# Performance work log

Hardware: AMD Instinct MI355X
Metric: run time of the kernel (lower is better)

The kernel has to match this reference:

```python
import jax, jax.numpy as jnp
import numpy as np


def setup_inputs() -> dict:
    key = jax.random.key(0)
    # coeffs_tensor: stacked/padded wavelet coefficients [B, F, T]
    coeffs = jax.random.normal(key, (16, 256, 8192), dtype=jnp.float32)
    return {"coeffs": coeffs}


def reference(coeffs) -> jnp.ndarray:
    B, F, T = coeffs.shape
    # torch.angle on a real tensor -> 0 for x>=0, pi for x<0; jnp.angle matches.
    phase = jnp.angle(coeffs)
    inst_freq = jnp.diff(phase, axis=-1)
    inst_freq = jnp.pad(inst_freq, ((0, 0), (0, 0), (0, 1)))  # F.pad(..., (0,1))
    freq_adjusted = jnp.clip(inst_freq, -1.0, 1.0)  # [B,F,T]
    # k = (f + freq_adjusted).long(); .long() truncates toward zero, as does astype(int32)
    f_idx = jnp.arange(F, dtype=coeffs.dtype)[None, :, None]
    k = jnp.clip((f_idx + freq_adjusted).astype(jnp.int32), 0, F - 1)  # [B,F,T]
    # Fused scatter-add over all (b, f, t): sst[b, k[b,f,t], t] += coeffs[b, f, t]
    b_idx = jnp.arange(B)[:, None, None]
    t_idx = jnp.arange(T)[None, None, :]
    sst = jnp.zeros_like(coeffs).at[b_idx, k, t_idx].add(coeffs)
    return sst
```

## Files before the change

### kernel.cpp

```cpp
#include <hip/hip_runtime.h>

#define BB 16
#define FF 256
#define TT 8192
#define F_CHUNK 16
#define THREADS 256

__device__ __forceinline__ int sgn_bit(float x) {
    return (int)(__float_as_uint(x) >> 31);
}

struct Raw { float4 v; float e; };

__global__ __launch_bounds__(THREADS) void sst_kernel(const float* __restrict__ in,
                                                      float* __restrict__ out) {
    const int t    = blockIdx.x * (THREADS * 4) + threadIdx.x * 4;
    const int fs   = blockIdx.y * F_CHUNK;
    const int b    = blockIdx.z;
    const int lane = threadIdx.x & 63;

    const float* src = in  + (size_t)b * FF * TT + t;
    float*       dst = out + (size_t)b * FF * TT + t;

    const bool tail = (t + 4 >= TT);

    auto load_raw = [&](int f) {
        Raw r;
        r.v = *reinterpret_cast<const float4*>(src + (size_t)f * TT);
        r.e = (lane == 63 && !tail) ? src[(size_t)f * TT + 4] : 0.0f;
        return r;
    };
    auto adj_of = [&](const Raw& r) {
        float nxt = __shfl_down(r.v.x, 1, 64);
        if (lane == 63) nxt = r.e;
        const int s0 = sgn_bit(r.v.x), s1 = sgn_bit(r.v.y), s2 = sgn_bit(r.v.z),
                  s3 = sgn_bit(r.v.w), s4 = sgn_bit(nxt);
        int4 a;
        a.x = s1 - s0;
        a.y = s2 - s1;
        a.z = s3 - s2;
        a.w = tail ? 0 : (s4 - s3);
        return a;
    };

    float4 vprev, vcur, vnext;
    int4   aprev, acur, anext;
    Raw    rn, rn2;

    if (fs == 0) {
        aprev = make_int4(9, 9, 9, 9);
        vprev = make_float4(0.f, 0.f, 0.f, 0.f);
    } else {
        Raw r = load_raw(fs - 1);
        vprev = r.v; aprev = adj_of(r);
    }
    {
        Raw r = load_raw(fs);
        vcur = r.v; acur = adj_of(r);
    }
    rn = load_raw(fs + 1);

    #pragma unroll
    for (int i = 0; i < F_CHUNK; ++i) {
        const int g = fs + i;

        const bool want2 = (i + 2 <= F_CHUNK) && (g + 2 < FF);
        if (want2) rn2 = load_raw(g + 2);

        if (g + 1 < FF) {
            vnext = rn.v; anext = adj_of(rn);
        } else {
            anext = make_int4(9, 9, 9, 9);
            vnext = make_float4(0.f, 0.f, 0.f, 0.f);
        }

        const bool isFirst = (g == 0);
        const bool isLast  = (g == FF - 1);

        float4 r;
        {
            const bool bc = (acur.x == 0) || (isFirst && acur.x < 0) || (isLast && acur.x > 0);
            r.x = ((aprev.x == 1) ? vprev.x : 0.f) + (bc ? vcur.x : 0.f)
                + ((anext.x == -1) ? vnext.x : 0.f);
        }
        {
            const bool bc = (acur.y == 0) || (isFirst && acur.y < 0) || (isLast && acur.y > 0);
            r.y = ((aprev.y == 1) ? vprev.y : 0.f) + (bc ? vcur.y : 0.f)
                + ((anext.y == -1) ? vnext.y : 0.f);
        }
        {
            const bool bc = (acur.z == 0) || (isFirst && acur.z < 0) || (isLast && acur.z > 0);
            r.z = ((aprev.z == 1) ? vprev.z : 0.f) + (bc ? vcur.z : 0.f)
                + ((anext.z == -1) ? vnext.z : 0.f);
        }
        {
            const bool bc = (acur.w == 0) || (isFirst && acur.w < 0) || (isLast && acur.w > 0);
            r.w = ((aprev.w == 1) ? vprev.w : 0.f) + (bc ? vcur.w : 0.f)
                + ((anext.w == -1) ? vnext.w : 0.f);
        }

        *reinterpret_cast<float4*>(dst + (size_t)g * TT) = r;

        vprev = vcur;  aprev = acur;
        vcur  = vnext; acur  = anext;
        rn    = rn2;
    }
}

extern "C" void kernel_launch(void* const* d_in, const int* in_sizes, int n_in,
                              void* d_out, int out_size, void* d_ws, size_t ws_size,
                              hipStream_t stream) {
    const float* in  = (const float*)d_in[0];
    float*       out = (float*)d_out;
    dim3 grid(TT / (THREADS * 4), FF / F_CHUNK, BB);
    sst_kernel<<<grid, THREADS, 0, stream>>>(in, out);
}
```

Baseline: 240.9 us.

## Widen per-thread time span to 8, pack sign bits, use nontemporal stores

Each thread now covers 8 time steps using two float4 loads and keeps the per-row phase-change data as a packed 9-bit sign mask instead of int4 vectors. Output is written with nontemporal vector stores so the write stream skips the caches. F_CHUNK is halved to 8 and launch bounds request 8 waves per SIMD to keep occupancy up. The halo reloads per chunk (rows fs-1 and fs+1) now make up a larger share of input traffic, and register pressure rises with the wider per-thread tile.

```diff
diff --git a/kernel.cpp b/kernel.cpp
--- a/kernel.cpp
+++ b/kernel.cpp
@@ -3,107 +3,101 @@
 #define BB 16
 #define FF 256
 #define TT 8192
-#define F_CHUNK 16
+#define F_CHUNK 8
 #define THREADS 256
+#define PT 8
 
-__device__ __forceinline__ int sgn_bit(float x) {
-    return (int)(__float_as_uint(x) >> 31);
-}
+typedef float f32x4 __attribute__((ext_vector_type(4)));
 
-struct Raw { float4 v; float e; };
+__device__ __forceinline__ unsigned sbit(float x) { return __float_as_uint(x) >> 31u; }
 
-__global__ __launch_bounds__(THREADS) void sst_kernel(const float* __restrict__ in,
-                                                      float* __restrict__ out) {
-    const int t    = blockIdx.x * (THREADS * 4) + threadIdx.x * 4;
+struct Raw { float4 a, b; float e; };
+struct Row { float v[PT]; unsigned s; };
+
+__global__ __launch_bounds__(THREADS, 8) void sst_kernel(const float* __restrict__ in,
+                                                         float* __restrict__ out) {
+    const int t0   = blockIdx.x * (THREADS * PT) + threadIdx.x * PT;
     const int fs   = blockIdx.y * F_CHUNK;
     const int b    = blockIdx.z;
     const int lane = threadIdx.x & 63;
+    const bool tail = (t0 + PT >= TT);
 
-    const float* src = in  + (size_t)b * FF * TT + t;
-    float*       dst = out + (size_t)b * FF * TT + t;
-
-    const bool tail = (t + 4 >= TT);
+    const float* src = in  + (size_t)b * FF * TT + t0;
+    float*       dst = out + (size_t)b * FF * TT + t0;
 
     auto load_raw = [&](int f) {
         Raw r;
-        r.v = *reinterpret_cast<const float4*>(src + (size_t)f * TT);
-        r.e = (lane == 63 && !tail) ? src[(size_t)f * TT + 4] : 0.0f;
+        const float* p = src + (size_t)f * TT;
+        r.a = *reinterpret_cast<const float4*>(p);
+        r.b = *reinterpret_cast<const float4*>(p + 4);
+        r.e = (lane == 63 && !tail) ? p[PT] : 0.0f;
         return r;
     };
-    auto adj_of = [&](const Raw& r) {
-        float nxt = __shfl_down(r.v.x, 1, 64);
+    auto finish = [&](const Raw& r) {
+        Row w;
+        float nxt = __shfl_down(r.a.x, 1, 64);
         if (lane == 63) nxt = r.e;
-        const int s0 = sgn_bit(r.v.x), s1 = sgn_bit(r.v.y), s2 = sgn_bit(r.v.z),
-                  s3 = sgn_bit(r.v.w), s4 = sgn_bit(nxt);
-        int4 a;
-        a.x = s1 - s0;
-        a.y = s2 - s1;
-        a.z = s3 - s2;
-        a.w = tail ? 0 : (s4 - s3);
-        return a;
+        unsigned s = sbit(r.a.x)        | (sbit(r.a.y) << 1) | (sbit(r.a.z) << 2)
+                   | (sbit(r.a.w) << 3) | (sbit(r.b.x) << 4) | (sbit(r.b.y) << 5)
+                   | (sbit(r.b.z) << 6) | (sbit(r.b.w) << 7) | (sbit(nxt)   << 8);
+        if (tail) s = (s & 0xFFu) | ((s & 0x80u) << 1);
+        w.s = s;
+        w.v[0] = r.a.x; w.v[1] = r.a.y; w.v[2] = r.a.z; w.v[3] = r.a.w;
+        w.v[4] = r.b.x; w.v[5] = r.b.y; w.v[6] = r.b.z; w.v[7] = r.b.w;
+        return w;
     };
 
-    float4 vprev, vcur, vnext;
-    int4   aprev, acur, anext;
-    Raw    rn, rn2;
+    Row rprev, rcur, rnext;
+    Raw rn, rn2;
 
     if (fs == 0) {
-        aprev = make_int4(9, 9, 9, 9);
-        vprev = make_float4(0.f, 0.f, 0.f, 0.f);
+        rprev.s = 0u;
+        #pragma unroll
+        for (int j = 0; j < PT; ++j) rprev.v[j] = 0.f;
     } else {
-        Raw r = load_raw(fs - 1);
-        vprev = r.v; aprev = adj_of(r);
+        rprev = finish(load_raw(fs - 1));
     }
-    {
-        Raw r = load_raw(fs);
-        vcur = r.v; acur = adj_of(r);
-    }
+    rcur = finish(load_raw(fs));
     rn = load_raw(fs + 1);
 
     #pragma unroll
     for (int i = 0; i < F_CHUNK; ++i) {
         const int g = fs + i;
 
-        const bool want2 = (i + 2 <= F_CHUNK) && (g + 2 < FF);
-        if (want2) rn2 = load_raw(g + 2);
+        if (i + 2 <= F_CHUNK && g + 2 < FF) rn2 = load_raw(g + 2);
 
         if (g + 1 < FF) {
-            vnext = rn.v; anext = adj_of(rn);
+            rnext = finish(rn);
         } else {
-            anext = make_int4(9, 9, 9, 9);
-            vnext = make_float4(0.f, 0.f, 0.f, 0.f);
+            rnext.s = 0u;
+            #pragma unroll
+            for (int j = 0; j < PT; ++j) rnext.v[j] = 0.f;
         }
 
         const bool isFirst = (g == 0);
         const bool isLast  = (g == FF - 1);
 
-        float4 r;
-        {
-            const bool bc = (acur.x == 0) || (isFirst && acur.x < 0) || (isLast && acur.x > 0);
-            r.x = ((aprev.x == 1) ? vprev.x : 0.f) + (bc ? vcur.x : 0.f)
-                + ((anext.x == -1) ? vnext.x : 0.f);
-        }
-        {
-            const bool bc = (acur.y == 0) || (isFirst && acur.y < 0) || (isLast && acur.y > 0);
-            r.y = ((aprev.y == 1) ? vprev.y : 0.f) + (bc ? vcur.y : 0.f)
-                + ((anext.y == -1) ? vnext.y : 0.f);
-        }
-        {
-            const bool bc = (acur.z == 0) || (isFirst && acur.z < 0) || (isLast && acur.z > 0);
-            r.z = ((aprev.z == 1) ? vprev.z : 0.f) + (bc ? vcur.z : 0.f)
-                + ((anext.z == -1) ? vnext.z : 0.f);
-        }
-        {
-            const bool bc = (acur.w == 0) || (isFirst && acur.w < 0) || (isLast && acur.w > 0);
-            r.w = ((aprev.w == 1) ? vprev.w : 0.f) + (bc ? vcur.w : 0.f)
-                + ((anext.w == -1) ? vnext.w : 0.f);
+        float r[PT];
+        #pragma unroll
+        for (int j = 0; j < PT; ++j) {
+            const unsigned xp = (rprev.s >> j) & 3u;
+            const unsigned xc = (rcur.s  >> j) & 3u;
+            const unsigned xn = (rnext.s >> j) & 3u;
+            const bool bc = (xc == 0u) || (xc == 3u)
+                          || (isFirst && xc == 1u)
+                          || (isLast  && xc == 2u);
+            r[j] = ((xp == 2u) ? rprev.v[j] : 0.f)
+                 + (bc          ? rcur.v[j]  : 0.f)
+                 + ((xn == 1u)  ? rnext.v[j] : 0.f);
         }
 
-        *reinterpret_cast<float4*>(dst + (size_t)g * TT) = r;
+        f32x4 o0 = { r[0], r[1], r[2], r[3] };
+        f32x4 o1 = { r[4], r[5], r[6], r[7] };
+        f32x4* dp = reinterpret_cast<f32x4*>(dst + (size_t)g * TT);
+        __builtin_nontemporal_store(o0, dp);
+        __builtin_nontemporal_store(o1, dp + 1);
 
-        vprev = vcur;  aprev = acur;
-        vcur  = vnext; acur  = anext;
-        rn    = rn2;
+        rprev = rcur; rcur = rnext; rn = rn2;
     }
 }
 
@@ -112,6 +106,6 @@
                               hipStream_t stream) {
     const float* in  = (const float*)d_in[0];
     float*       out = (float*)d_out;
-    dim3 grid(TT / (THREADS * 4), FF / F_CHUNK, BB);
+    dim3 grid(TT / (THREADS * PT), FF / F_CHUNK, BB);
     sst_kernel<<<grid, THREADS, 0, stream>>>(in, out);
 }
```

Measured after the change: 248.4 us. 1.03x slower.
